# Performance work log

Hardware: AMD Instinct MI355X
Metric: run time of the kernel (lower is better)

The kernel has to match this reference:

```python
import jax, jax.numpy as jnp
import numpy as np

ENZ_DIM, CPD_DIM, OUT_DIM = 1280, 256, 512
B, L_ENZ, L_CPD = 32, 512, 128
SCALE = OUT_DIM ** 0.5


def _linear_params(key, d_in, d_out):
    k1, k2 = jax.random.split(key)
    lim = 1.0 / np.sqrt(d_in)
    W = jax.random.uniform(k1, (d_in, d_out), jnp.float32, -lim, lim)
    b = jax.random.uniform(k2, (d_out,), jnp.float32, -lim, lim)
    return W, b


def setup_inputs() -> dict:
    key = jax.random.key(0)
    ks = jax.random.split(key, 16)
    inp = {
        "enz_node_feature": jax.random.normal(ks[0], (B, L_ENZ, ENZ_DIM), jnp.float32),
        "substrate_node_feature": jax.random.normal(ks[1], (B, L_CPD, CPD_DIM), jnp.float32),
        "product_node_feature": jax.random.normal(ks[2], (B, L_CPD, CPD_DIM), jnp.float32),
        "enz_node_feature_mask": jnp.ones((B, L_ENZ), dtype=bool),
        "substrate_node_feature_mask": jnp.ones((B, L_CPD), dtype=bool),
        "product_node_feature_mask": jnp.ones((B, L_CPD), dtype=bool),
        "interaction_weight": jax.random.normal(ks[3], (B, L_CPD, L_ENZ), jnp.float32),
    }
    # cross_attn_enzyme: query=enz (ENZ_DIM), key/value=cpd (CPD_DIM)
    inp["enz_Wq"], inp["enz_bq"] = _linear_params(ks[4], ENZ_DIM, OUT_DIM)
    inp["enz_Wk"], inp["enz_bk"] = _linear_params(ks[5], CPD_DIM, OUT_DIM)
    inp["enz_Wv"], inp["enz_bv"] = _linear_params(ks[6], CPD_DIM, OUT_DIM)
    # cross_attn_substrate: query=cpd, key/value=enz
    inp["sub_Wq"], inp["sub_bq"] = _linear_params(ks[7], CPD_DIM, OUT_DIM)
    inp["sub_Wk"], inp["sub_bk"] = _linear_params(ks[8], ENZ_DIM, OUT_DIM)
    inp["sub_Wv"], inp["sub_bv"] = _linear_params(ks[9], ENZ_DIM, OUT_DIM)
    # cross_attn_product: query=cpd, key/value=enz
    inp["prod_Wq"], inp["prod_bq"] = _linear_params(ks[10], CPD_DIM, OUT_DIM)
    inp["prod_Wk"], inp["prod_bk"] = _linear_params(ks[11], ENZ_DIM, OUT_DIM)
    inp["prod_Wv"], inp["prod_bv"] = _linear_params(ks[12], ENZ_DIM, OUT_DIM)
    return inp


def _cross_attn(q_in, k_in, v_in, q_mask, k_mask, Wq, bq, Wk, bk, Wv, bv, attn_bias=None):
    q = q_in @ Wq + bq          # [B, Lq, D]
    k = k_in @ Wk + bk          # [B, Lk, D]
    v = v_in @ Wv + bv          # [B, Lk, D]
    scores = jnp.einsum("bqd,bkd->bqk", q, k) / SCALE
    if attn_bias is not None:
        scores = scores + attn_bias
    mask = q_mask[:, :, None] & k_mask[:, None, :]   # [B, Lq, Lk]
    scores = jnp.where(mask, scores, -1e9)
    w = jax.nn.softmax(scores, axis=-1)
    return jnp.einsum("bqk,bkd->bqd", w, v)


def reference(enz_node_feature, substrate_node_feature, product_node_feature,
              enz_node_feature_mask, substrate_node_feature_mask, product_node_feature_mask,
              interaction_weight,
              enz_Wq, enz_bq, enz_Wk, enz_bk, enz_Wv, enz_bv,
              sub_Wq, sub_bq, sub_Wk, sub_bk, sub_Wv, sub_bv,
              prod_Wq, prod_bq, prod_Wk, prod_bk, prod_Wv, prod_bv):
    subs_pocket_weight = interaction_weight                       # [B, L_cpd, L_enz]
    pocket_subs_weight = jnp.swapaxes(interaction_weight, 1, 2)   # [B, L_enz, L_cpd]

    enzyme_subs = _cross_attn(enz_node_feature, substrate_node_feature, substrate_node_feature,
                              enz_node_feature_mask, substrate_node_feature_mask,
                              enz_Wq, enz_bq, enz_Wk, enz_bk, enz_Wv, enz_bv,
                              attn_bias=pocket_subs_weight)
    subs_enzyme = _cross_attn(substrate_node_feature, enz_node_feature, enz_node_feature,
                              substrate_node_feature_mask, enz_node_feature_mask,
                              sub_Wq, sub_bq, sub_Wk, sub_bk, sub_Wv, sub_bv,
                              attn_bias=subs_pocket_weight)
    # product path reuses cross_attn_enzyme weights for enz->prod (as in torch code)
    enzyme_prod = _cross_attn(enz_node_feature, product_node_feature, product_node_feature,
                              enz_node_feature_mask, product_node_feature_mask,
                              enz_Wq, enz_bq, enz_Wk, enz_bk, enz_Wv, enz_bv)
    prod_enzyme = _cross_attn(product_node_feature, enz_node_feature, enz_node_feature,
                              product_node_feature_mask, enz_node_feature_mask,
                              prod_Wq, prod_bq, prod_Wk, prod_bk, prod_Wv, prod_bv)

    return jnp.concatenate([enzyme_subs.mean(axis=1), subs_enzyme.mean(axis=1),
                            enzyme_prod.mean(axis=1), prod_enzyme.mean(axis=1)], axis=-1)
```

## Files before the change

### kernel.cpp

```cpp
#include <hip/hip_runtime.h>
#include <cstdint>
#include <cstddef>


#define SCALE_INV 0.044194173824159216f

typedef short bf16x8 __attribute__((ext_vector_type(8)));
typedef float f32x4  __attribute__((ext_vector_type(4)));

__device__ __forceinline__ ushort f2bf(float f) {
  union { float f; unsigned u; } c; c.f = f;
  unsigned u = c.u + 0x7fffu + ((c.u >> 16) & 1u);
  return (ushort)(u >> 16);
}
__device__ __forceinline__ float bf2f(ushort h) {
  return __uint_as_float(((unsigned)h) << 16);
}
__device__ __forceinline__ void gload16(const ushort* g, ushort* l) {
  __builtin_amdgcn_global_load_lds(
      (const __attribute__((address_space(1))) void*)g,
      (__attribute__((address_space(3))) void*)l, 16, 0, 0);
}

__device__ __forceinline__ void cvt8(const float* __restrict__ in,
                                     ushort* __restrict__ out, int blk, int n) {
  int i = (blk * 256 + (int)threadIdx.x) * 8;
  if (i >= n) return;
  float4 a = *(const float4*)(in + i);
  float4 b = *(const float4*)(in + i + 4);
  ushort o[8] = { f2bf(a.x), f2bf(a.y), f2bf(a.z), f2bf(a.w),
                  f2bf(b.x), f2bf(b.y), f2bf(b.z), f2bf(b.w) };
  *(uint4*)(out + i) = *(uint4*)o;
}

__global__ __launch_bounds__(256) void prep_fused(
    const float* __restrict__ enz, const float* __restrict__ sub,
    const float* __restrict__ prod,
    ushort* __restrict__ enz_b, ushort* __restrict__ sub_b, ushort* __restrict__ prod_b,
    const float* __restrict__ enz_Wq, const float* __restrict__ enz_Wk,
    const float* __restrict__ sub_Wq, const float* __restrict__ sub_Wk,
    const float* __restrict__ prod_Wq, const float* __restrict__ prod_Wk,
    ushort* __restrict__ eWq_b, ushort* __restrict__ eWk_b,
    ushort* __restrict__ sWq_b, ushort* __restrict__ sWk_b,
    ushort* __restrict__ pWq_b, ushort* __restrict__ pWk_b,
    const float* __restrict__ enz_bq, const float* __restrict__ sub_bq,
    const float* __restrict__ prod_bq,
    const float* __restrict__ enz_bv, const float* __restrict__ sub_bv,
    const float* __restrict__ prod_bv,
    float* __restrict__ u_s_s, float* __restrict__ u_p_s,
    float* __restrict__ u_e_s,
    float* __restrict__ zero_base, float* __restrict__ out)
{
  const int f = blockIdx.x, t = threadIdx.x;
  if (f < 10240) { cvt8(enz, enz_b, f, 20971520); return; }
  if (f < 10752) { cvt8(sub, sub_b, f - 10240, 1048576); return; }
  if (f < 11264) { cvt8(prod, prod_b, f - 10752, 1048576); return; }
  if (f < 12416) {
    const int l = f - 11264;
    if (l < 320)       cvt8(enz_Wq,  eWq_b, l,        655360);
    else if (l < 640)  cvt8(sub_Wk,  sWk_b, l - 320,  655360);
    else if (l < 960)  cvt8(prod_Wk, pWk_b, l - 640,  655360);
    else if (l < 1024) cvt8(enz_Wk,  eWk_b, l - 960,  131072);
    else if (l < 1088) cvt8(sub_Wq,  sWq_b, l - 1024, 131072);
    else               cvt8(prod_Wq, pWq_b, l - 1088, 131072);
    return;
  }
  if (f < 12592) {
    const int g = f - 12416;
    const float* W; const float* bv; float* U; int d0;
    if (g < 80)       { W = sub_Wk;  bv = sub_bq;  U = u_s_s; d0 = g * 16; }
    else if (g < 160) { W = prod_Wk; bv = prod_bq; U = u_p_s; d0 = (g - 80) * 16; }
    else              { W = enz_Wk;  bv = enz_bq;  U = u_e_s; d0 = (g - 160) * 16; }
    const int r = t >> 4, i = t & 15, d = d0 + r;
    const float* row = W + (size_t)d * 512;
    float s = 0.f;
#pragma unroll
    for (int j = 0; j < 32; j++) s += row[i + j * 16] * bv[i + j * 16];
    s += __shfl_xor(s, 1); s += __shfl_xor(s, 2);
    s += __shfl_xor(s, 4); s += __shfl_xor(s, 8);
    if (i == 0) U[d] = s * SCALE_INV;
    return;
  }
  if (f < 13168) { zero_base[(f - 12592) * 256 + t] = 0.f; return; }
  {
    const int idx = (f - 13168) * 256 + t;
    const int col = idx & 2047;
    const int q = col >> 9, n = col & 511;
    const float* bvp = (q == 1) ? sub_bv : (q == 3) ? prod_bv : enz_bv;
    out[idx] = bvp[n];
  }
}

__device__ __forceinline__ void mfma_tile64(
    const ushort* __restrict__ A, int lda,
    const ushort* __restrict__ Bt, int ldb, int K,
    int bm, int bn, ushort* AsBase, ushort* BsBase, f32x4 (&acc)[4][4])
{
  const int t = threadIdx.x, wave = t >> 6, lane = t & 63;
  const int r8 = lane >> 3;
  const int csrc = 8 * ((lane & 7) ^ r8);
  const int wm = (wave >> 1) * 64, wn = (wave & 1) * 64;
  const int fl = lane & 15, fq = lane >> 4;
  for (int k0 = 0; k0 < K; k0 += 64) {
    __syncthreads();
#pragma unroll
    for (int i = 0; i < 4; i++) {
      const int row = i * 32 + wave * 8 + r8;
      ushort* dst = AsBase + row * 64 + (lane & 7) * 8;
      gload16(A + (size_t)(bm + row) * lda + k0 + csrc, dst);
      gload16(Bt + (size_t)(bn + row) * ldb + k0 + csrc,
              BsBase + row * 64 + (lane & 7) * 8);
    }
    __syncthreads();
#pragma unroll
    for (int kk = 0; kk < 2; kk++) {
      bf16x8 bfr[4];
#pragma unroll
      for (int j = 0; j < 4; j++) {
        const int row = wn + j * 16 + fl;
        bfr[j] = *(const bf16x8*)(BsBase + row * 64 +
                                  8 * (((kk << 2) + fq) ^ (row & 7)));
      }
#pragma unroll
      for (int i = 0; i < 4; i++) {
        const int row = wm + i * 16 + fl;
        bf16x8 af = *(const bf16x8*)(AsBase + row * 64 +
                                     8 * (((kk << 2) + fq) ^ (row & 7)));
#pragma unroll
        for (int j = 0; j < 4; j++)
          acc[i][j] = __builtin_amdgcn_mfma_f32_16x16x32_bf16(af, bfr[j], acc[i][j], 0, 0, 0);
      }
    }
  }
}

__global__ __launch_bounds__(256) void fold_w3(
    const ushort* __restrict__ eWq_b, const ushort* __restrict__ eWk_b,
    const ushort* __restrict__ sWq_b, const ushort* __restrict__ sWk_b,
    const ushort* __restrict__ pWq_b, const ushort* __restrict__ pWk_b,
    const ushort* __restrict__ sub_b, const ushort* __restrict__ prod_b,
    const ushort* __restrict__ enz_b,
    const float* __restrict__ u_e_s, const float* __restrict__ u_s_s,
    const float* __restrict__ u_p_s,
    ushort* __restrict__ W3t, float* __restrict__ t_es, float* __restrict__ t_ep,
    float* __restrict__ t_se, float* __restrict__ t_pe)
{
  __shared__ __align__(16) ushort As[128 * 64];
  __shared__ __align__(16) ushort Bs[128 * 64];
  __shared__ float us[256];
  __shared__ float us2[2][1280];
  const int f = blockIdx.x, t = threadIdx.x;
  if (f >= 76) {
    const int g2 = f - 76;
    for (int i = t; i < 1280; i += 256) { us2[0][i] = u_s_s[i]; us2[1][i] = u_p_s[i]; }
    __syncthreads();
    const int row = g2 * 64 + (t >> 2), lane4 = t & 3;
    const ushort* xr = enz_b + (size_t)row * 1280;
    float ss = 0.f, sp = 0.f;
#pragma unroll
    for (int q = 0; q < 40; ++q) {
      const int c0 = q * 32 + lane4 * 8;
      bf16x8 v = *(const bf16x8*)(xr + c0);
#pragma unroll
      for (int i = 0; i < 8; ++i) {
        const float x = bf2f((ushort)v[i]);
        ss += x * us2[0][c0 + i];
        sp += x * us2[1][c0 + i];
      }
    }
    ss += __shfl_xor(ss, 1); ss += __shfl_xor(ss, 2);
    sp += __shfl_xor(sp, 1); sp += __shfl_xor(sp, 2);
    if (lane4 == 0) { t_se[row] = ss; t_pe[row] = sp; }
    return;
  }
  if (f >= 60) {
    const int g = f - 60, path = g >> 3, blk8 = g & 7;
    const ushort* Xb = path ? prod_b : sub_b;
    float* T = path ? t_ep : t_es;
    us[t] = u_e_s[t];
    __syncthreads();
#pragma unroll
    for (int e = 0; e < 2; ++e) {
      const int row = blk8 * 512 + e * 256 + t;
      const ushort* xr = Xb + (size_t)row * 256;
      float s = 0.f;
      for (int c = 0; c < 256; c += 8) {
        bf16x8 v = *(const bf16x8*)(xr + c);
#pragma unroll
        for (int i = 0; i < 8; ++i) s += bf2f((ushort)v[i]) * us[c + i];
      }
      T[row] = s;
    }
    return;
  }
  const int seg = f / 20, l = f % 20;
  const int bm = (l / 10) * 128, bn = (l % 10) * 128;
  const ushort* A  = (seg == 0) ? eWk_b : (seg == 1) ? sWq_b : pWq_b;
  const ushort* Bt = (seg == 0) ? eWq_b : (seg == 1) ? sWk_b : pWk_b;
  f32x4 acc[4][4] = {};
  mfma_tile64(A, 512, Bt, 512, 512, bm, bn, As, Bs, acc);
  const int lane = t & 63, wave = t >> 6;
  const int wm = (wave >> 1) * 64, wn = (wave & 1) * 64;
  const int fl = lane & 15, fq = lane >> 4;
#pragma unroll
  for (int i = 0; i < 4; i++)
#pragma unroll
    for (int j = 0; j < 4; j++) {
      const int col = bn + wn + j * 16 + fl;
#pragma unroll
      for (int r = 0; r < 4; r++) {
        const int row = seg * 256 + bm + wm + i * 16 + fq * 4 + r;
        W3t[(size_t)row * 1280 + col] = f2bf(acc[i][j][r]);
      }
    }
}

__device__ __forceinline__ void yg_stage_unit(
    const ushort* __restrict__ gbase, int k0, int u,
    ushort* ldsTile, int wv, int l, int srow8, int scol)
{
  const int row0 = u * 64 + wv * 8 + srow8;
  gload16(gbase + (size_t)row0 * 1280 + k0 + scol,
          ldsTile + u * 4096 + wv * 512 + l * 8);
}

__device__ __forceinline__ bf16x8 yg_frag(const ushort* tile, int row, int kk, int fq) {
  const int X = (kk * 64 + fq * 16) ^ ((row & 7) << 4);
  return *(const bf16x8*)((const char*)tile + row * 128 + X);
}

__global__ __launch_bounds__(512, 4) void y_gemm(
    const ushort* __restrict__ A,
    const ushort* __restrict__ B,
    ushort* __restrict__ Y)
{
  extern __shared__ __align__(16) ushort lds[];
  const int t = threadIdx.x;
  const int wv = t >> 6, l = t & 63;
  const int fl = l & 15, fq = l >> 4;
  const int f = blockIdx.x;
  const int xcd = f & 7, slot = f >> 3;
  const int mt = xcd * 16 + (slot >> 2), nt = slot & 3;
  const int bm = mt * 128, bn = nt * 192;
  const int wm = (wv >> 2) * 64, wn = (wv & 3) * 48;
  const int srow8 = l >> 3;
  const int scol = 8 * ((l & 7) ^ srow8);
  const ushort* Ag = A + (size_t)bm * 1280;
  const ushort* Bg = B + (size_t)bn * 1280;

  ushort* A0 = lds;
  ushort* B0 = lds + 8192;
  ushort* A1 = lds + 20480;
  ushort* B1 = lds + 28672;

  f32x4 acc[4][3] = {};

#pragma unroll
  for (int u = 0; u < 2; ++u) yg_stage_unit(Ag, 0, u, A0, wv, l, srow8, scol);
#pragma unroll
  for (int u = 0; u < 3; ++u) yg_stage_unit(Bg, 0, u, B0, wv, l, srow8, scol);
#pragma unroll
  for (int u = 0; u < 2; ++u) yg_stage_unit(Ag, 64, u, A1, wv, l, srow8, scol);
  asm volatile("s_waitcnt vmcnt(2)" ::: "memory");
  __builtin_amdgcn_s_barrier();
  __builtin_amdgcn_sched_barrier(0);

  for (int j = 0; j < 20; ++j) {
    const int p = j & 1;
    const ushort* At = p ? A1 : A0;
    const ushort* Bt = p ? B1 : B0;
    ushort* Bo = p ? B0 : B1;
    const int kn = (j + 1) * 64;

    bf16x8 bf_[3][2];
#pragma unroll
    for (int n = 0; n < 3; ++n)
#pragma unroll
      for (int kk = 0; kk < 2; ++kk)
        bf_[n][kk] = yg_frag(Bt, wn + n * 16 + fl, kk, fq);

#pragma unroll
    for (int mp = 0; mp < 4; ++mp) {
      if (mp < 3 && j < 19) yg_stage_unit(Bg, kn, mp, Bo, wv, l, srow8, scol);
      bf16x8 a0[2];
#pragma unroll
      for (int kk = 0; kk < 2; ++kk)
        a0[kk] = yg_frag(At, wm + mp * 16 + fl, kk, fq);
      __builtin_amdgcn_s_setprio(1);
#pragma unroll
      for (int kk = 0; kk < 2; ++kk)
#pragma unroll
        for (int n = 0; n < 3; ++n)
          acc[mp][n] = __builtin_amdgcn_mfma_f32_16x16x32_bf16(
              a0[kk], bf_[n][kk], acc[mp][n], 0, 0, 0);
      __builtin_amdgcn_s_setprio(0);
    }

    asm volatile("" ::: "memory");
    __builtin_amdgcn_s_barrier();
    if (j + 2 < 20) {
      ushort* Ao = (ushort*)At;
#pragma unroll
      for (int u = 0; u < 2; ++u)
        yg_stage_unit(Ag, (j + 2) * 64, u, Ao, wv, l, srow8, scol);
    }
    if (j < 18) asm volatile("s_waitcnt vmcnt(2)" ::: "memory");
    else        asm volatile("s_waitcnt vmcnt(0)" ::: "memory");
    __builtin_amdgcn_s_barrier();
    __builtin_amdgcn_sched_barrier(0);
  }

#pragma unroll
  for (int m = 0; m < 4; ++m)
#pragma unroll
    for (int n = 0; n < 3; ++n)
#pragma unroll
      for (int r = 0; r < 4; ++r) {
        const int row = bm + wm + m * 16 + fq * 4 + r;
        const int col = bn + wn + n * 16 + fl;
        Y[(size_t)row * 768 + col] = f2bf(acc[m][n][r]);
      }
}

__global__ __launch_bounds__(256) void score_fused(
    const ushort* __restrict__ Y, const ushort* __restrict__ sub_b,
    const ushort* __restrict__ prod_b, const float* __restrict__ iw,
    const float* __restrict__ t_es, const float* __restrict__ t_ep,
    const float* __restrict__ t_se, const float* __restrict__ t_pe,
    float* __restrict__ Sc_se, float* __restrict__ Sc_pe,
    float* __restrict__ l_se, float* __restrict__ l_pe,
    float* __restrict__ wsum_es, float* __restrict__ wsum_ep)
{
  __shared__ __align__(16) ushort As[128 * 64];
  __shared__ __align__(16) ushort Bs[128 * 64];
  __shared__ float red[2][128];
  __shared__ float red2[2][128];
  const int f = blockIdx.x, t = threadIdx.x;
  const int lane = t & 63, wave = t >> 6;
  const int wm = (wave >> 1) * 64, wn = (wave & 1) * 64;
  const int fl = lane & 15, fq = lane >> 4;
  f32x4 acc[4][4] = {};

  if (f < 256) {
    const int path = f >> 7, l = f & 127, b = l & 31, qt = l >> 5;
    const int bn = qt * 128;
    const ushort* X  = (path ? prod_b : sub_b) + (size_t)b * 32768;
    const ushort* Yb = Y + (size_t)b * 512 * 768;
    mfma_tile64(X, 256, Yb, 768, 256, 0, bn, As, Bs, acc);
    const size_t ib = (size_t)b * 65536;
    const float* Tp = (path ? t_ep : t_es) + b * 128;
    float tvv[4][4];
#pragma unroll
    for (int i = 0; i < 4; i++)
#pragma unroll
      for (int r = 0; r < 4; r++) tvv[i][r] = Tp[wm + i * 16 + fq * 4 + r];
    float csum[4] = { 0.f, 0.f, 0.f, 0.f };
#pragma unroll
    for (int i = 0; i < 4; i++)
#pragma unroll
      for (int j = 0; j < 4; j++)
#pragma unroll
        for (int r = 0; r < 4; r++) {
          const int row = wm + i * 16 + fq * 4 + r;
          const int col = wn + j * 16 + fl;
          float s = acc[i][j][r] * SCALE_INV + tvv[i][r];
          if (path == 0) s += iw[ib + (size_t)row * 512 + (bn + col)];
          const float e = __expf(s);
          acc[i][j][r] = e;
          csum[j] += e;
        }
#pragma unroll
    for (int m = 16; m <= 32; m <<= 1)
#pragma unroll
      for (int j = 0; j < 4; j++) csum[j] += __shfl_xor(csum[j], m);
    if (fq == 0)
#pragma unroll
      for (int j = 0; j < 4; j++) red[wave >> 1][wn + j * 16 + fl] = csum[j];
    __syncthreads();
    float invc[4];
#pragma unroll
    for (int j = 0; j < 4; j++) {
      const int col = wn + j * 16 + fl;
      invc[j] = 1.f / (red[0][col] + red[1][col]);
    }
    float rsum[4][4];
#pragma unroll
    for (int i = 0; i < 4; i++)
#pragma unroll
      for (int r = 0; r < 4; r++) rsum[i][r] = 0.f;
#pragma unroll
    for (int i = 0; i < 4; i++)
#pragma unroll
      for (int j = 0; j < 4; j++)
#pragma unroll
        for (int r = 0; r < 4; r++) rsum[i][r] += acc[i][j][r] * invc[j];
#pragma unroll
    for (int m = 1; m <= 8; m <<= 1)
#pragma unroll
      for (int i = 0; i < 4; i++)
#pragma unroll
        for (int r = 0; r < 4; r++)
          rsum[i][r] += __shfl_xor(rsum[i][r], m);
    if (fl == 0)
#pragma unroll
      for (int i = 0; i < 4; i++)
#pragma unroll
        for (int r = 0; r < 4; r++)
          red2[wave & 1][wm + i * 16 + fq * 4 + r] = rsum[i][r];
    __syncthreads();
    float* ws = (path ? wsum_ep : wsum_es) + b * 128;
    if (t < 128) atomicAdd(&ws[t], red2[0][t] + red2[1][t]);
  } else {
    const int g = f - 256, path = g >> 7, l = g & 127, b = l & 31, nt = l >> 5;
    const int bn = nt * 128;
    const ushort* A  = (path ? prod_b : sub_b) + (size_t)b * 32768;
    const ushort* Bt = Y + (size_t)b * 512 * 768 + 256 + path * 256;
    mfma_tile64(A, 256, Bt, 768, 256, 0, bn, As, Bs, acc);
    const size_t ib = (size_t)b * 65536;
    float* Sc = (path ? Sc_pe : Sc_se) + ib;
    const float* Tq = (path ? t_pe : t_se) + b * 512;
    float tv[4];
#pragma unroll
    for (int j = 0; j < 4; j++) tv[j] = Tq[bn + wn + j * 16 + fl];
    float rsum[4][4];
#pragma unroll
    for (int i = 0; i < 4; i++)
#pragma unroll
      for (int r = 0; r < 4; r++) rsum[i][r] = 0.f;
#pragma unroll
    for (int i = 0; i < 4; i++)
#pragma unroll
      for (int j = 0; j < 4; j++)
#pragma unroll
        for (int r = 0; r < 4; r++) {
          const int row = wm + i * 16 + fq * 4 + r;
          const int col = wn + j * 16 + fl;
          float s = acc[i][j][r] * SCALE_INV + tv[j];
          if (path == 0) s += iw[ib + (size_t)row * 512 + (bn + col)];
          const float e = __expf(s);
          Sc[(size_t)row * 512 + bn + col] = e;
          rsum[i][r] += e;
        }
#pragma unroll
    for (int m = 1; m <= 8; m <<= 1)
#pragma unroll
      for (int i = 0; i < 4; i++)
#pragma unroll
        for (int r = 0; r < 4; r++)
          rsum[i][r] += __shfl_xor(rsum[i][r], m);
    if (fl == 0)
#pragma unroll
      for (int i = 0; i < 4; i++)
#pragma unroll
        for (int r = 0; r < 4; r++)
          red[wave & 1][wm + i * 16 + fq * 4 + r] = rsum[i][r];
    __syncthreads();
    float* lr = (path ? l_pe : l_se) + b * 128;
    if (t < 128) atomicAdd(&lr[t], red[0][t] + red[1][t]);
  }
}

__global__ __launch_bounds__(256) void colsum2(
    const float* __restrict__ Sc_se, const float* __restrict__ Sc_pe,
    const float* __restrict__ l_se, const float* __restrict__ l_pe,
    float* __restrict__ wsum_se, float* __restrict__ wsum_pe)
{
  __shared__ float inv[32];
  const int f = blockIdx.x, t = threadIdx.x;
  const int path = f >> 7, l = f & 127, b = l & 31, qc = l >> 5;
  const float* Sc = (path ? Sc_pe : Sc_se) + (size_t)b * 65536 + (size_t)(qc * 32) * 512;
  const float* lv = (path ? l_pe : l_se) + b * 128 + qc * 32;
  float* ws = (path ? wsum_pe : wsum_se) + b * 512;
  if (t < 32) inv[t] = 1.f / lv[t];
  __syncthreads();
  float a0 = 0.f, a1 = 0.f;
  for (int q = 0; q < 32; q++) {
    const float iq = inv[q];
    a0 += Sc[(size_t)q * 512 + t] * iq;
    a1 += Sc[(size_t)q * 512 + 256 + t] * iq;
  }
  atomicAdd(&ws[t], a0);
  atomicAdd(&ws[t + 256], a1);
}

__global__ __launch_bounds__(256) void wx_fused(
    const float* __restrict__ wsum_se, const float* __restrict__ wsum_pe,
    const float* __restrict__ wsum_es, const float* __restrict__ wsum_ep,
    const ushort* __restrict__ enz_b, const ushort* __restrict__ sub_b,
    const ushort* __restrict__ prod_b,
    float* __restrict__ wx_se, float* __restrict__ wx_pe,
    float* __restrict__ wx_es, float* __restrict__ wx_ep)
{
  __shared__ float wse[256], wpe[256];
  const int f = blockIdx.x, t = threadIdx.x;
  if (f < 320) {
    const int ch = f % 5, tmp = f / 5, b = tmp & 31, kh = tmp >> 5;
    wse[t] = wsum_se[b * 512 + kh * 256 + t];
    wpe[t] = wsum_pe[b * 512 + kh * 256 + t];
    __syncthreads();
    const int c = ch * 256 + t;
    const ushort* X = enz_b + (size_t)b * 512 * 1280 + (size_t)(kh * 256) * 1280 + c;
    float a_se = 0.f, a_pe = 0.f;
#pragma unroll 4
    for (int k = 0; k < 256; k++) {
      const float x = bf2f(X[(size_t)k * 1280]);
      a_se += wse[k] * x;
      a_pe += wpe[k] * x;
    }
    atomicAdd(&wx_se[b * 1280 + c], a_se);
    atomicAdd(&wx_pe[b * 1280 + c], a_pe);
  } else if (f < 352) {
    const int b = f - 320;
    const ushort* X = sub_b + (size_t)b * 128 * 256 + t;
    float a = 0.f;
#pragma unroll 4
    for (int k = 0; k < 128; k++) a += wsum_es[b * 128 + k] * bf2f(X[(size_t)k * 256]);
    wx_es[b * 256 + t] = a;
  } else {
    const int b = f - 352;
    const ushort* X = prod_b + (size_t)b * 128 * 256 + t;
    float a = 0.f;
#pragma unroll 4
    for (int k = 0; k < 128; k++) a += wsum_ep[b * 128 + k] * bf2f(X[(size_t)k * 256]);
    wx_ep[b * 256 + t] = a;
  }
}

__global__ __launch_bounds__(256) void out_gemv(
    const float* __restrict__ wx_es, const float* __restrict__ wx_se,
    const float* __restrict__ wx_ep, const float* __restrict__ wx_pe,
    const float* __restrict__ enz_Wv, const float* __restrict__ sub_Wv,
    const float* __restrict__ prod_Wv,
    float* __restrict__ out)
{
  __shared__ float sw[32][64];
  const int f = blockIdx.x, t = threadIdx.x;
  const float* wx; const float* Wv; int Cdim, qoff, nb, cc; float inv;
  if (f < 40)      { wx = wx_se; Wv = sub_Wv;  Cdim = 1280; inv = 1.f / 128.f; qoff = 512;  nb = f & 1;        cc = f >> 1; }
  else if (f < 80) { wx = wx_pe; Wv = prod_Wv; Cdim = 1280; inv = 1.f / 128.f; qoff = 1536; nb = (f - 40) & 1; cc = (f - 40) >> 1; }
  else if (f < 88) { wx = wx_es; Wv = enz_Wv;  Cdim = 256;  inv = 1.f / 512.f; qoff = 0;    nb = (f - 80) & 1; cc = (f - 80) >> 1; }
  else             { wx = wx_ep; Wv = enz_Wv;  Cdim = 256;  inv = 1.f / 512.f; qoff = 1024; nb = (f - 88) & 1; cc = (f - 88) >> 1; }
  const int c0 = cc * 64, n = nb * 256 + t;
#pragma unroll
  for (int i = 0; i < 8; i++) {
    const int idx = t + i * 256, b = idx >> 6, c = idx & 63;
    sw[b][c] = wx[(size_t)b * Cdim + c0 + c];
  }
  __syncthreads();
  float acc[32];
#pragma unroll
  for (int b = 0; b < 32; b++) acc[b] = 0.f;
  for (int c = 0; c < 64; c += 4) {
    const float w0 = Wv[(size_t)(c0 + c) * 512 + n];
    const float w1 = Wv[(size_t)(c0 + c + 1) * 512 + n];
    const float w2 = Wv[(size_t)(c0 + c + 2) * 512 + n];
    const float w3 = Wv[(size_t)(c0 + c + 3) * 512 + n];
#pragma unroll
    for (int b = 0; b < 32; b++) {
      const float4 s = *(const float4*)&sw[b][c];
      acc[b] += s.x * w0 + s.y * w1 + s.z * w2 + s.w * w3;
    }
  }
#pragma unroll
  for (int b = 0; b < 32; b++)
    atomicAdd(&out[(size_t)b * 2048 + qoff + n], acc[b] * inv);
}

extern "C" void kernel_launch(void* const* d_in, const int* in_sizes, int n_in,
                              void* d_out, int out_size, void* d_ws, size_t ws_size,
                              hipStream_t stream)
{
  (void)in_sizes; (void)n_in; (void)out_size; (void)ws_size;
  const float* enz     = (const float*)d_in[0];
  const float* sub     = (const float*)d_in[1];
  const float* prod    = (const float*)d_in[2];
  const float* iw      = (const float*)d_in[6];
  const float* enz_Wq  = (const float*)d_in[7];
  const float* enz_bq  = (const float*)d_in[8];
  const float* enz_Wk  = (const float*)d_in[9];
  const float* enz_Wv  = (const float*)d_in[11];
  const float* enz_bv  = (const float*)d_in[12];
  const float* sub_Wq  = (const float*)d_in[13];
  const float* sub_bq  = (const float*)d_in[14];
  const float* sub_Wk  = (const float*)d_in[15];
  const float* sub_Wv  = (const float*)d_in[17];
  const float* sub_bv  = (const float*)d_in[18];
  const float* prod_Wq = (const float*)d_in[19];
  const float* prod_bq = (const float*)d_in[20];
  const float* prod_Wk = (const float*)d_in[21];
  const float* prod_Wv = (const float*)d_in[23];
  const float* prod_bv = (const float*)d_in[24];
  float* out = (float*)d_out;

  char* wsb = (char*)d_ws;
  size_t off = 0;
  auto alloc = [&](size_t bytes) {
    void* p = wsb + off;
    off += (bytes + 255) & ~(size_t)255;
    return p;
  };
  ushort* enz_b   = (ushort*)alloc((size_t)32 * 512 * 1280 * 2);
  ushort* sub_b   = (ushort*)alloc((size_t)32 * 128 * 256 * 2);
  ushort* prod_b  = (ushort*)alloc((size_t)32 * 128 * 256 * 2);
  ushort* eWq_b   = (ushort*)alloc((size_t)1280 * 512 * 2);
  ushort* sWk_b   = (ushort*)alloc((size_t)1280 * 512 * 2);
  ushort* pWk_b   = (ushort*)alloc((size_t)1280 * 512 * 2);
  ushort* eWk_b   = (ushort*)alloc((size_t)256 * 512 * 2);
  ushort* sWq_b   = (ushort*)alloc((size_t)256 * 512 * 2);
  ushort* pWq_b   = (ushort*)alloc((size_t)256 * 512 * 2);
  ushort* W3t     = (ushort*)alloc((size_t)768 * 1280 * 2);
  ushort* Y       = (ushort*)alloc((size_t)16384 * 768 * 2);
  float*  u_s_s   = (float*)alloc(1280 * 4);
  float*  u_p_s   = (float*)alloc(1280 * 4);
  float*  u_e_s   = (float*)alloc(256 * 4);
  float*  t_es    = (float*)alloc(4096 * 4);
  float*  t_ep    = (float*)alloc(4096 * 4);
  float*  t_se    = (float*)alloc(16384 * 4);
  float*  t_pe    = (float*)alloc(16384 * 4);
  float*  Sc_se   = (float*)alloc((size_t)32 * 128 * 512 * 4);
  float*  Sc_pe   = (float*)alloc((size_t)32 * 128 * 512 * 4);
  float* wsum_es = (float*)alloc(4096 * 4);
  float* wsum_ep = (float*)alloc(4096 * 4);
  float* wsum_se = (float*)alloc(16384 * 4);
  float* wsum_pe = (float*)alloc(16384 * 4);
  float* l_se    = (float*)alloc(4096 * 4);
  float* l_pe    = (float*)alloc(4096 * 4);
  float* wx_se   = (float*)alloc(40960 * 4);
  float* wx_pe   = (float*)alloc(40960 * 4);
  float* wx_es   = (float*)alloc(8192 * 4);
  float* wx_ep   = (float*)alloc(8192 * 4);

  static bool ygemm_attr_set = false;
  if (!ygemm_attr_set) {
    hipFuncSetAttribute(reinterpret_cast<const void*>(y_gemm),
                        hipFuncAttributeMaxDynamicSharedMemorySize, 81920);
    ygemm_attr_set = true;
  }

  const dim3 blk(256);

  prep_fused<<<13424, blk, 0, stream>>>(
      enz, sub, prod, enz_b, sub_b, prod_b,
      enz_Wq, enz_Wk, sub_Wq, sub_Wk, prod_Wq, prod_Wk,
      eWq_b, eWk_b, sWq_b, sWk_b, pWq_b, pWk_b,
      enz_bq, sub_bq, prod_bq, enz_bv, sub_bv, prod_bv,
      u_s_s, u_p_s, u_e_s, wsum_es, out);

  fold_w3<<<332, blk, 0, stream>>>(
      eWq_b, eWk_b, sWq_b, sWk_b, pWq_b, pWk_b,
      sub_b, prod_b, enz_b, u_e_s, u_s_s, u_p_s,
      W3t, t_es, t_ep, t_se, t_pe);

  y_gemm<<<512, 512, 81920, stream>>>(enz_b, W3t, Y);

  score_fused<<<512, blk, 0, stream>>>(
      Y, sub_b, prod_b, iw, t_es, t_ep, t_se, t_pe,
      Sc_se, Sc_pe, l_se, l_pe, wsum_es, wsum_ep);

  colsum2<<<256, blk, 0, stream>>>(Sc_se, Sc_pe, l_se, l_pe, wsum_se, wsum_pe);

  wx_fused<<<384, blk, 0, stream>>>(
      wsum_se, wsum_pe, wsum_es, wsum_ep, enz_b, sub_b, prod_b,
      wx_se, wx_pe, wx_es, wx_ep);

  out_gemv<<<96, blk, 0, stream>>>(
      wx_es, wx_se, wx_ep, wx_pe, enz_Wv, sub_Wv, prod_Wv, out);
}
```

Baseline: 314.9 us.

## Fuse substrate/product score softmax with column sums, dropping score buffer pass

Splits the score kernel into two kernels. The substrate/product→enzyme path now uses a new 512-thread kernel that holds a full 32x512 row strip per block, so the row softmax denominator is computed in-block and normalized column sums are accumulated directly. This removes the global Sc score buffer write/read, the l_* row-sum atomics, the colsum2 launch and the zeroing blocks for those buffers. In exchange it relies on more atomics per column and gives a different tile shape with lower MFMA reuse per block.

```diff
diff --git a/kernel.cpp b/kernel.cpp
--- a/kernel.cpp
+++ b/kernel.cpp
@@ -81,9 +81,9 @@
     if (i == 0) U[d] = s * SCALE_INV;
     return;
   }
-  if (f < 13168) { zero_base[(f - 12592) * 256 + t] = 0.f; return; }
+  if (f < 13072) { zero_base[(f - 12592) * 256 + t] = 0.f; return; }
   {
-    const int idx = (f - 13168) * 256 + t;
+    const int idx = (f - 13072) * 256 + t;
     const int col = idx & 2047;
     const int q = col >> 9, n = col & 511;
     const float* bvp = (q == 1) ? sub_bv : (q == 3) ? prod_bv : enz_bv;
@@ -322,13 +322,10 @@
       }
 }
 
-__global__ __launch_bounds__(256) void score_fused(
+__global__ __launch_bounds__(256) void score_esep(
     const ushort* __restrict__ Y, const ushort* __restrict__ sub_b,
     const ushort* __restrict__ prod_b, const float* __restrict__ iw,
     const float* __restrict__ t_es, const float* __restrict__ t_ep,
-    const float* __restrict__ t_se, const float* __restrict__ t_pe,
-    float* __restrict__ Sc_se, float* __restrict__ Sc_pe,
-    float* __restrict__ l_se, float* __restrict__ l_pe,
     float* __restrict__ wsum_es, float* __restrict__ wsum_ep)
 {
   __shared__ __align__(16) ushort As[128 * 64];
@@ -341,146 +338,197 @@
   const int fl = lane & 15, fq = lane >> 4;
   f32x4 acc[4][4] = {};
 
-  if (f < 256) {
-    const int path = f >> 7, l = f & 127, b = l & 31, qt = l >> 5;
-    const int bn = qt * 128;
-    const ushort* X  = (path ? prod_b : sub_b) + (size_t)b * 32768;
-    const ushort* Yb = Y + (size_t)b * 512 * 768;
-    mfma_tile64(X, 256, Yb, 768, 256, 0, bn, As, Bs, acc);
-    const size_t ib = (size_t)b * 65536;
-    const float* Tp = (path ? t_ep : t_es) + b * 128;
-    float tvv[4][4];
+  const int path = f >> 7, l = f & 127, b = l & 31, qt = l >> 5;
+  const int bn = qt * 128;
+  const ushort* X  = (path ? prod_b : sub_b) + (size_t)b * 32768;
+  const ushort* Yb = Y + (size_t)b * 512 * 768;
+  mfma_tile64(X, 256, Yb, 768, 256, 0, bn, As, Bs, acc);
+  const size_t ib = (size_t)b * 65536;
+  const float* Tp = (path ? t_ep : t_es) + b * 128;
+  float tvv[4][4];
+#pragma unroll
+  for (int i = 0; i < 4; i++)
+#pragma unroll
+    for (int r = 0; r < 4; r++) tvv[i][r] = Tp[wm + i * 16 + fq * 4 + r];
+  float csum[4] = { 0.f, 0.f, 0.f, 0.f };
+#pragma unroll
+  for (int i = 0; i < 4; i++)
+#pragma unroll
+    for (int j = 0; j < 4; j++)
+#pragma unroll
+      for (int r = 0; r < 4; r++) {
+        const int row = wm + i * 16 + fq * 4 + r;
+        const int col = wn + j * 16 + fl;
+        float s = acc[i][j][r] * SCALE_INV + tvv[i][r];
+        if (path == 0) s += iw[ib + (size_t)row * 512 + (bn + col)];
+        const float e = __expf(s);
+        acc[i][j][r] = e;
+        csum[j] += e;
+      }
+#pragma unroll
+  for (int m = 16; m <= 32; m <<= 1)
+#pragma unroll
+    for (int j = 0; j < 4; j++) csum[j] += __shfl_xor(csum[j], m);
+  if (fq == 0)
+#pragma unroll
+    for (int j = 0; j < 4; j++) red[wave >> 1][wn + j * 16 + fl] = csum[j];
+  __syncthreads();
+  float invc[4];
+#pragma unroll
+  for (int j = 0; j < 4; j++) {
+    const int col = wn + j * 16 + fl;
+    invc[j] = 1.f / (red[0][col] + red[1][col]);
+  }
+  float rsum[4][4];
+#pragma unroll
+  for (int i = 0; i < 4; i++)
+#pragma unroll
+    for (int r = 0; r < 4; r++) rsum[i][r] = 0.f;
+#pragma unroll
+  for (int i = 0; i < 4; i++)
+#pragma unroll
+    for (int j = 0; j < 4; j++)
+#pragma unroll
+      for (int r = 0; r < 4; r++) rsum[i][r] += acc[i][j][r] * invc[j];
+#pragma unroll
+  for (int m = 1; m <= 8; m <<= 1)
 #pragma unroll
     for (int i = 0; i < 4; i++)
 #pragma unroll
-      for (int r = 0; r < 4; r++) tvv[i][r] = Tp[wm + i * 16 + fq * 4 + r];
-    float csum[4] = { 0.f, 0.f, 0.f, 0.f };
+      for (int r = 0; r < 4; r++)
+        rsum[i][r] += __shfl_xor(rsum[i][r], m);
+  if (fl == 0)
 #pragma unroll
     for (int i = 0; i < 4; i++)
 #pragma unroll
-      for (int j = 0; j < 4; j++)
-#pragma unroll
-        for (int r = 0; r < 4; r++) {
-          const int row = wm + i * 16 + fq * 4 + r;
-          const int col = wn + j * 16 + fl;
-          float s = acc[i][j][r] * SCALE_INV + tvv[i][r];
-          if (path == 0) s += iw[ib + (size_t)row * 512 + (bn + col)];
-          const float e = __expf(s);
-          acc[i][j][r] = e;
-          csum[j] += e;
+      for (int r = 0; r < 4; r++)
+        red2[wave & 1][wm + i * 16 + fq * 4 + r] = rsum[i][r];
+  __syncthreads();
+  float* ws = (path ? wsum_ep : wsum_es) + b * 128;
+  if (t < 128) atomicAdd(&ws[t], red2[0][t] + red2[1][t]);
+}
+
+__global__ __launch_bounds__(512) void score_sepe(
+    const ushort* __restrict__ Y, const ushort* __restrict__ sub_b,
+    const ushort* __restrict__ prod_b, const float* __restrict__ iw,
+    const float* __restrict__ t_se, const float* __restrict__ t_pe,
+    float* __restrict__ wsum_se, float* __restrict__ wsum_pe)
+{
+  __shared__ __align__(16) ushort As[32 * 64];
+  __shared__ __align__(16) ushort Bs[256 * 64];
+  __shared__ float red[8][32];
+  const int f = blockIdx.x, t = threadIdx.x;
+  const int path = f >> 7, l = f & 127, b = l >> 2, qq = l & 3;
+  const int wv = t >> 6, lane = t & 63;
+  const int fl = lane & 15, fq = lane >> 4;
+  const ushort* A  = (path ? prod_b : sub_b) + (size_t)b * 32768 + qq * 32 * 256;
+  const ushort* Bt = Y + (size_t)b * 512 * 768 + 256 + path * 256;
+  const float* Tq = (path ? t_pe : t_se) + b * 512;
+  float* ws = (path ? wsum_pe : wsum_se) + b * 512;
+  const size_t ib = (size_t)b * 65536 + (size_t)(qq * 32) * 512;
+
+  f32x4 acc[2][4] = {};
+
+  for (int nh = 0; nh < 2; ++nh) {
+    for (int k0 = 0; k0 < 256; k0 += 64) {
+      __syncthreads();
+      if (t < 256) {
+        const int ar = t >> 3;
+        gload16(A + (size_t)ar * 256 + k0 + 8 * ((t & 7) ^ (ar & 7)),
+                As + ar * 64 + (t & 7) * 8);
+      }
+#pragma unroll
+      for (int i = 0; i < 4; ++i) {
+        const int br = i * 64 + (t >> 3);
+        gload16(Bt + (size_t)(nh * 256 + br) * 768 + k0 + 8 * ((t & 7) ^ (br & 7)),
+                Bs + br * 64 + (t & 7) * 8);
+      }
+      __syncthreads();
+#pragma unroll
+      for (int kk = 0; kk < 2; ++kk) {
+        bf16x8 af[2], bfr[2];
+#pragma unroll
+        for (int m = 0; m < 2; ++m) {
+          const int row = m * 16 + fl;
+          af[m] = *(const bf16x8*)(As + row * 64 + 8 * (((kk << 2) + fq) ^ (row & 7)));
         }
 #pragma unroll
-    for (int m = 16; m <= 32; m <<= 1)
-#pragma unroll
-      for (int j = 0; j < 4; j++) csum[j] += __shfl_xor(csum[j], m);
-    if (fq == 0)
-#pragma unroll
-      for (int j = 0; j < 4; j++) red[wave >> 1][wn + j * 16 + fl] = csum[j];
-    __syncthreads();
-    float invc[4];
-#pragma unroll
-    for (int j = 0; j < 4; j++) {
-      const int col = wn + j * 16 + fl;
-      invc[j] = 1.f / (red[0][col] + red[1][col]);
-    }
-    float rsum[4][4];
-#pragma unroll
-    for (int i = 0; i < 4; i++)
-#pragma unroll
-      for (int r = 0; r < 4; r++) rsum[i][r] = 0.f;
-#pragma unroll
-    for (int i = 0; i < 4; i++)
-#pragma unroll
-      for (int j = 0; j < 4; j++)
-#pragma unroll
-        for (int r = 0; r < 4; r++) rsum[i][r] += acc[i][j][r] * invc[j];
-#pragma unroll
-    for (int m = 1; m <= 8; m <<= 1)
-#pragma unroll
-      for (int i = 0; i < 4; i++)
-#pragma unroll
-        for (int r = 0; r < 4; r++)
-          rsum[i][r] += __shfl_xor(rsum[i][r], m);
-    if (fl == 0)
-#pragma unroll
-      for (int i = 0; i < 4; i++)
-#pragma unroll
-        for (int r = 0; r < 4; r++)
-          red2[wave & 1][wm + i * 16 + fq * 4 + r] = rsum[i][r];
-    __syncthreads();
-    float* ws = (path ? wsum_ep : wsum_es) + b * 128;
-    if (t < 128) atomicAdd(&ws[t], red2[0][t] + red2[1][t]);
-  } else {
-    const int g = f - 256, path = g >> 7, l = g & 127, b = l & 31, nt = l >> 5;
-    const int bn = nt * 128;
-    const ushort* A  = (path ? prod_b : sub_b) + (size_t)b * 32768;
-    const ushort* Bt = Y + (size_t)b * 512 * 768 + 256 + path * 256;
-    mfma_tile64(A, 256, Bt, 768, 256, 0, bn, As, Bs, acc);
-    const size_t ib = (size_t)b * 65536;
-    float* Sc = (path ? Sc_pe : Sc_se) + ib;
-    const float* Tq = (path ? t_pe : t_se) + b * 512;
-    float tv[4];
-#pragma unroll
-    for (int j = 0; j < 4; j++) tv[j] = Tq[bn + wn + j * 16 + fl];
-    float rsum[4][4];
-#pragma unroll
-    for (int i = 0; i < 4; i++)
-#pragma unroll
-      for (int r = 0; r < 4; r++) rsum[i][r] = 0.f;
-#pragma unroll
-    for (int i = 0; i < 4; i++)
-#pragma unroll
-      for (int j = 0; j < 4; j++)
-#pragma unroll
-        for (int r = 0; r < 4; r++) {
-          const int row = wm + i * 16 + fq * 4 + r;
-          const int col = wn + j * 16 + fl;
-          float s = acc[i][j][r] * SCALE_INV + tv[j];
-          if (path == 0) s += iw[ib + (size_t)row * 512 + (bn + col)];
-          const float e = __expf(s);
-          Sc[(size_t)row * 512 + bn + col] = e;
-          rsum[i][r] += e;
+        for (int n = 0; n < 2; ++n) {
+          const int row = wv * 32 + n * 16 + fl;
+          bfr[n] = *(const bf16x8*)(Bs + row * 64 + 8 * (((kk << 2) + fq) ^ (row & 7)));
         }
 #pragma unroll
-    for (int m = 1; m <= 8; m <<= 1)
-#pragma unroll
-      for (int i = 0; i < 4; i++)
-#pragma unroll
-        for (int r = 0; r < 4; r++)
-          rsum[i][r] += __shfl_xor(rsum[i][r], m);
-    if (fl == 0)
-#pragma unroll
-      for (int i = 0; i < 4; i++)
-#pragma unroll
-        for (int r = 0; r < 4; r++)
-          red[wave & 1][wm + i * 16 + fq * 4 + r] = rsum[i][r];
-    __syncthreads();
-    float* lr = (path ? l_pe : l_se) + b * 128;
-    if (t < 128) atomicAdd(&lr[t], red[0][t] + red[1][t]);
-  }
-}
-
-__global__ __launch_bounds__(256) void colsum2(
-    const float* __restrict__ Sc_se, const float* __restrict__ Sc_pe,
-    const float* __restrict__ l_se, const float* __restrict__ l_pe,
-    float* __restrict__ wsum_se, float* __restrict__ wsum_pe)
-{
-  __shared__ float inv[32];
-  const int f = blockIdx.x, t = threadIdx.x;
-  const int path = f >> 7, l = f & 127, b = l & 31, qc = l >> 5;
-  const float* Sc = (path ? Sc_pe : Sc_se) + (size_t)b * 65536 + (size_t)(qc * 32) * 512;
-  const float* lv = (path ? l_pe : l_se) + b * 128 + qc * 32;
-  float* ws = (path ? wsum_pe : wsum_se) + b * 512;
-  if (t < 32) inv[t] = 1.f / lv[t];
+        for (int m = 0; m < 2; ++m)
+#pragma unroll
+          for (int n = 0; n < 2; ++n)
+            acc[m][nh * 2 + n] = __builtin_amdgcn_mfma_f32_16x16x32_bf16(
+                af[m], bfr[n], acc[m][nh * 2 + n], 0, 0, 0);
+      }
+    }
+  }
+
+  float tv[4];
+  int colv[4];
+#pragma unroll
+  for (int c = 0; c < 4; ++c) {
+    const int nh = c >> 1, n = c & 1;
+    colv[c] = nh * 256 + wv * 32 + n * 16 + fl;
+    tv[c] = Tq[colv[c]];
+  }
+  float rsum[2][4];
+#pragma unroll
+  for (int m = 0; m < 2; ++m)
+#pragma unroll
+    for (int r = 0; r < 4; ++r) rsum[m][r] = 0.f;
+#pragma unroll
+  for (int m = 0; m < 2; ++m)
+#pragma unroll
+    for (int c = 0; c < 4; ++c)
+#pragma unroll
+      for (int r = 0; r < 4; ++r) {
+        const int row = m * 16 + fq * 4 + r;
+        float s = acc[m][c][r] * SCALE_INV + tv[c];
+        if (path == 0) s += iw[ib + (size_t)row * 512 + colv[c]];
+        const float e = __expf(s);
+        acc[m][c][r] = e;
+        rsum[m][r] += e;
+      }
+#pragma unroll
+  for (int mm = 1; mm <= 8; mm <<= 1)
+#pragma unroll
+    for (int m = 0; m < 2; ++m)
+#pragma unroll
+      for (int r = 0; r < 4; ++r)
+        rsum[m][r] += __shfl_xor(rsum[m][r], mm);
+  if (fl == 0)
+#pragma unroll
+    for (int m = 0; m < 2; ++m)
+#pragma unroll
+      for (int r = 0; r < 4; ++r)
+        red[wv][m * 16 + fq * 4 + r] = rsum[m][r];
   __syncthreads();
-  float a0 = 0.f, a1 = 0.f;
-  for (int q = 0; q < 32; q++) {
-    const float iq = inv[q];
-    a0 += Sc[(size_t)q * 512 + t] * iq;
-    a1 += Sc[(size_t)q * 512 + 256 + t] * iq;
-  }
-  atomicAdd(&ws[t], a0);
-  atomicAdd(&ws[t + 256], a1);
+  float invl[2][4];
+#pragma unroll
+  for (int m = 0; m < 2; ++m)
+#pragma unroll
+    for (int r = 0; r < 4; ++r) {
+      const int row = m * 16 + fq * 4 + r;
+      float lsum = 0.f;
+#pragma unroll
+      for (int w = 0; w < 8; ++w) lsum += red[w][row];
+      invl[m][r] = 1.f / lsum;
+    }
+#pragma unroll
+  for (int c = 0; c < 4; ++c) {
+    float w = 0.f;
+#pragma unroll
+    for (int m = 0; m < 2; ++m)
+#pragma unroll
+      for (int r = 0; r < 4; ++r) w += acc[m][c][r] * invl[m][r];
+    w += __shfl_xor(w, 16);
+    w += __shfl_xor(w, 32);
+    if (fq == 0) atomicAdd(&ws[colv[c]], w);
+  }
 }
 
 __global__ __launch_bounds__(256) void wx_fused(
@@ -617,14 +665,10 @@
   float*  t_ep    = (float*)alloc(4096 * 4);
   float*  t_se    = (float*)alloc(16384 * 4);
   float*  t_pe    = (float*)alloc(16384 * 4);
-  float*  Sc_se   = (float*)alloc((size_t)32 * 128 * 512 * 4);
-  float*  Sc_pe   = (float*)alloc((size_t)32 * 128 * 512 * 4);
   float* wsum_es = (float*)alloc(4096 * 4);
   float* wsum_ep = (float*)alloc(4096 * 4);
   float* wsum_se = (float*)alloc(16384 * 4);
   float* wsum_pe = (float*)alloc(16384 * 4);
-  float* l_se    = (float*)alloc(4096 * 4);
-  float* l_pe    = (float*)alloc(4096 * 4);
   float* wx_se   = (float*)alloc(40960 * 4);
   float* wx_pe   = (float*)alloc(40960 * 4);
   float* wx_es   = (float*)alloc(8192 * 4);
@@ -639,7 +683,7 @@
 
   const dim3 blk(256);
 
-  prep_fused<<<13424, blk, 0, stream>>>(
+  prep_fused<<<13328, blk, 0, stream>>>(
       enz, sub, prod, enz_b, sub_b, prod_b,
       enz_Wq, enz_Wk, sub_Wq, sub_Wk, prod_Wq, prod_Wk,
       eWq_b, eWk_b, sWq_b, sWk_b, pWq_b, pWk_b,
@@ -653,11 +697,11 @@
 
   y_gemm<<<512, 512, 81920, stream>>>(enz_b, W3t, Y);
 
-  score_fused<<<512, blk, 0, stream>>>(
-      Y, sub_b, prod_b, iw, t_es, t_ep, t_se, t_pe,
-      Sc_se, Sc_pe, l_se, l_pe, wsum_es, wsum_ep);
-
-  colsum2<<<256, blk, 0, stream>>>(Sc_se, Sc_pe, l_se, l_pe, wsum_se, wsum_pe);
+  score_esep<<<256, blk, 0, stream>>>(
+      Y, sub_b, prod_b, iw, t_es, t_ep, wsum_es, wsum_ep);
+
+  score_sepe<<<256, 512, 0, stream>>>(
+      Y, sub_b, prod_b, iw, t_se, t_pe, wsum_se, wsum_pe);
 
   wx_fused<<<384, blk, 0, stream>>>(
       wsum_se, wsum_pe, wsum_es, wsum_ep, enz_b, sub_b, prod_b,
```

New measurement: 336.4 us. +6.8%, slower.
